# Optimization experiments

Hardware: AMD Instinct MI355X
Metric: run time of the kernel (lower is better)

Reference implementation:

```python
import jax, jax.numpy as jnp
import numpy as np

EPS = 1e-9

def setup_inputs() -> dict:
    key = jax.random.key(0)
    ks = jax.random.split(key, 6)
    B, S, D, F, E, K = 2, 2048, 1024, 4096, 8, 2
    hidden = jax.random.normal(ks[0], (B, S, D), dtype=jnp.float32)
    expert_indices = jax.random.randint(ks[1], (B, S, K), 0, E, dtype=jnp.int32)
    expert_weights = jax.random.uniform(ks[2], (B, S, K), dtype=jnp.float32)
    # normalize like a real top-k router would
    expert_weights = expert_weights / jnp.sum(expert_weights, axis=-1, keepdims=True)
    router_logits = jax.random.normal(ks[3], (B, S, E), dtype=jnp.float32)
    w1 = jax.random.normal(ks[4], (E, D, F), dtype=jnp.float32) * (1.0 / np.sqrt(D))
    b1 = jnp.zeros((E, F), dtype=jnp.float32)
    w2 = jax.random.normal(ks[5], (E, F, D), dtype=jnp.float32) * (1.0 / np.sqrt(F))
    b2 = jnp.zeros((E, D), dtype=jnp.float32)
    return {"hidden": hidden, "expert_indices": expert_indices,
            "expert_weights": expert_weights, "router_logits": router_logits,
            "w1": w1, "b1": b1, "w2": w2, "b2": b2}

def reference(hidden, expert_indices, expert_weights, router_logits, w1, b1, w2, b2):
    # All-expert dense compute (faithful to torch.stack([expert(hidden) ...], dim=-2))
    # hidden: [B,S,D]; w1: [E,D,F]; w2: [E,F,D]
    h1 = jnp.einsum('bsd,edf->bsef', hidden, w1) + b1            # [B,S,E,F]
    h1 = jax.nn.gelu(h1)
    expert_outputs = jnp.einsum('bsef,efd->bsed', h1, w2) + b2   # [B,S,E,D]
    # gather selected experts along expert axis (torch.gather dim=-2)
    idx = expert_indices[..., None]                              # [B,S,K,1]
    selected = jnp.take_along_axis(expert_outputs, idx, axis=-2) # [B,S,K,D]
    mixed = jnp.sum(selected * expert_weights[..., None], axis=-2)  # [B,S,D]
    # observation stats
    route_probs = jax.nn.softmax(router_logits, axis=-1)
    log_p = jnp.log(jnp.clip(route_probs, EPS, None))
    route_entropy = jnp.mean(jnp.sum(-route_probs * log_p, axis=-1))
    top2 = jax.lax.top_k(route_probs, 2)[0]
    winner_margin = jnp.mean(top2[..., 0] - top2[..., -1])
    return (mixed, route_entropy, winner_margin)
```

## Files before the change

kernel.cpp:

```cpp
#include <hip/hip_runtime.h>
#include <stddef.h>
#include <stdint.h>

#define BDIM 2
#define SDIM 2048
#define DDIM 1024
#define FDIM 4096
#define ENUM 8
#define KSEL 2
#define TTOK (BDIM * SDIM)
#define PPAIR (TTOK * KSEL)
#define VOUT ((size_t)TTOK * DDIM)

typedef float f32x4 __attribute__((ext_vector_type(4)));
typedef short bf16x8 __attribute__((ext_vector_type(8)));
typedef unsigned short u16x8 __attribute__((ext_vector_type(8)));
typedef unsigned short u16x4 __attribute__((ext_vector_type(4)));

#define WAITV(N) asm volatile("s_waitcnt vmcnt(" #N ")" ::: "memory")
#define BARX() asm volatile("s_barrier" ::: "memory")

__device__ __forceinline__ unsigned short f2bf(float f) {
  unsigned int u = __float_as_uint(f);
  u += 0x7fffu + ((u >> 16) & 1u);
  return (unsigned short)(u >> 16);
}

__device__ __forceinline__ float gelu_tanh(float x) {
  float u = 0.7978845608028654f * (x + 0.044715f * x * x * x);
  float e = __expf(2.0f * u);
  float t = 1.0f - 2.0f / (e + 1.0f);
  return 0.5f * x * (1.0f + t);
}

__device__ __forceinline__ void gload16(const void* g, void* l) {
  __builtin_amdgcn_global_load_lds(
      (const __attribute__((address_space(1))) unsigned int*)g,
      (__attribute__((address_space(3))) unsigned int*)l, 16, 0, 0);
}

__global__ __launch_bounds__(256) void pre_kernel(const float* __restrict__ hidden,
                                                  unsigned short* __restrict__ hB,
                                                  const float* __restrict__ lg,
                                                  float* __restrict__ pst,
                                                  const int* __restrict__ eidx,
                                                  int* __restrict__ g_cnt,
                                                  int* __restrict__ g_off,
                                                  int* __restrict__ pairTok,
                                                  int* __restrict__ inv,
                                                  int* __restrict__ b256E,
                                                  int* __restrict__ b256M,
                                                  int* __restrict__ b128E,
                                                  int* __restrict__ b128M,
                                                  int* __restrict__ nT) {
  const int b = blockIdx.x;
  const int tid = threadIdx.x;
  if (b < 2048) {
    const int i = b * 256 + tid;
    f32x4 a = ((const f32x4*)hidden)[(size_t)i * 2];
    f32x4 c = ((const f32x4*)hidden)[(size_t)i * 2 + 1];
    u16x8 o;
    o[0] = f2bf(a[0]); o[1] = f2bf(a[1]); o[2] = f2bf(a[2]); o[3] = f2bf(a[3]);
    o[4] = f2bf(c[0]); o[5] = f2bf(c[1]); o[6] = f2bf(c[2]); o[7] = f2bf(c[3]);
    ((u16x8*)hB)[i] = o;
    return;
  }
  if (b < 2064) {
    __shared__ float se[256], sm[256];
    const int r = (b - 2048) * 256 + tid;
    float v[ENUM];
    float mx = -1e30f;
#pragma unroll
    for (int i = 0; i < ENUM; ++i) { v[i] = lg[r * ENUM + i]; mx = fmaxf(mx, v[i]); }
    float s = 0.f;
#pragma unroll
    for (int i = 0; i < ENUM; ++i) { v[i] = __expf(v[i] - mx); s += v[i]; }
    float invs = 1.f / s;
    float p1 = -1.f, p2 = -1.f, e_ = 0.f;
#pragma unroll
    for (int i = 0; i < ENUM; ++i) {
      float p = v[i] * invs;
      e_ -= p * logf(fmaxf(p, 1e-9f));
      if (p > p1) { p2 = p1; p1 = p; } else if (p > p2) { p2 = p; }
    }
    se[tid] = e_; sm[tid] = p1 - p2;
    __syncthreads();
    for (int st = 128; st > 0; st >>= 1) {
      if (tid < (unsigned)st) { se[tid] += se[tid + st]; sm[tid] += sm[tid + st]; }
      __syncthreads();
    }
    if (tid == 0) { pst[(b - 2048) * 2] = se[0]; pst[(b - 2048) * 2 + 1] = sm[0]; }
    return;
  }
  __shared__ int sc[ENUM], so[ENUM], scur[ENUM];
  if (tid < ENUM) sc[tid] = 0;
  __syncthreads();
  for (int p = tid; p < PPAIR; p += 256) atomicAdd(&sc[eidx[p]], 1);
  __syncthreads();
  if (tid == 0) {
    int o = 0, n256 = 0, n128 = 0;
    for (int e = 0; e < ENUM; ++e) {
      so[e] = o;
      const int cnt = sc[e];
      const int nf = cnt >> 8;
      const int rem = cnt - (nf << 8);
      for (int i = 0; i < nf; ++i) { b256E[n256] = e; b256M[n256] = i << 8; ++n256; }
      const int np = (rem + 127) >> 7;
      for (int j = 0; j < np; ++j) { b128E[n128] = e; b128M[n128] = (nf << 8) + (j << 7); ++n128; }
      o += cnt;
    }
    nT[0] = n256; nT[1] = n128;
  }
  __syncthreads();
  if (tid < ENUM) { scur[tid] = so[tid]; g_cnt[tid] = sc[tid]; g_off[tid] = so[tid]; }
  __syncthreads();
  for (int p = tid; p < PPAIR; p += 256) {
    int e = eidx[p];
    int pos = atomicAdd(&scur[e], 1);
    pairTok[pos] = p >> 1;
    inv[p] = pos;
  }
}

__global__ void statsB_kernel(const float* __restrict__ pst, float* __restrict__ out) {
  if (threadIdx.x == 0) {
    float a = 0.f, b = 0.f;
    for (int i = 0; i < 16; ++i) { a += pst[2 * i]; b += pst[2 * i + 1]; }
    out[VOUT]     = a / (float)TTOK;
    out[VOUT + 1] = b / (float)TTOK;
  }
}

__global__ __launch_bounds__(256) void transpose2_kernel(const float* __restrict__ w1,
                                                         unsigned short* __restrict__ w1T,
                                                         const float* __restrict__ w2,
                                                         unsigned short* __restrict__ w2T) {
  __shared__ float tile[64][65];
  const int z = blockIdx.y;
  const int b = blockIdx.x;
  const float* ip; unsigned short* op; int R, C, r0, c0;
  if (z < 8) {
    const size_t base = (size_t)z * DDIM * FDIM;
    ip = w1 + base; op = w1T + base; R = DDIM; C = FDIM;
    r0 = (b >> 6) << 6; c0 = (b & 63) << 6;
  } else {
    const size_t base = (size_t)(z - 8) * DDIM * FDIM;
    ip = w2 + base; op = w2T + base; R = FDIM; C = DDIM;
    r0 = (b & 63) << 6; c0 = (b >> 6) << 6;
  }
  const int tid = threadIdx.x;
  const int rr = tid >> 4;
  const int cc = (tid & 15) << 2;
#pragma unroll
  for (int k = 0; k < 4; ++k) {
    f32x4 v = *(const f32x4*)(ip + (size_t)(r0 + rr + 16 * k) * C + c0 + cc);
    tile[rr + 16 * k][cc + 0] = v[0];
    tile[rr + 16 * k][cc + 1] = v[1];
    tile[rr + 16 * k][cc + 2] = v[2];
    tile[rr + 16 * k][cc + 3] = v[3];
  }
  __syncthreads();
  const int oc = tid >> 3;
  const int ob = (tid & 7) << 3;
#pragma unroll
  for (int k = 0; k < 2; ++k) {
    const int c = oc + 32 * k;
    u16x8 o;
#pragma unroll
    for (int j = 0; j < 8; ++j) o[j] = f2bf(tile[ob + j][c]);
    *(u16x8*)(op + (size_t)(c0 + c) * R + r0 + ob) = o;
  }
}

__global__ __launch_bounds__(512, 2) void gemm1_fused(const unsigned short* __restrict__ hB,
                                                      const unsigned short* __restrict__ w1T,
                                                      const float* __restrict__ b1,
                                                      const int* __restrict__ g_cnt,
                                                      const int* __restrict__ g_off,
                                                      const int* __restrict__ pairTok,
                                                      const int* __restrict__ b256E,
                                                      const int* __restrict__ b256M,
                                                      const int* __restrict__ b128E,
                                                      const int* __restrict__ b128M,
                                                      const int* __restrict__ nT,
                                                      unsigned short* __restrict__ h1) {
  __shared__ __align__(16) char smem[131072];
  const int flat = blockIdx.x + 48 * blockIdx.y;
  const int w = (flat & 7) * 96 + (flat >> 3);
  const int mIdx = w % 48;
  const int nB = w / 48;
  const int n0 = nB << 8;

  const int tid = threadIdx.x;
  const int lane = tid & 63;
  const int wm = (tid >> 6) >> 2;
  const int wn = (tid >> 6) & 3;
  const int kh = lane >> 4;
  const int l15 = lane & 15;

  if (mIdx < 32) {
    if (mIdx >= nT[0]) return;
    const int e = b256E[mIdx];
    const int m0 = b256M[mIdx];
    const int off_e = g_off[e];

    const unsigned short* gArow[2];
    const unsigned short* gBrow[2];
    int ldsOff[2];
#pragma unroll
    for (int c = 0; c < 2; ++c) {
      const int idx = c * 512 + tid;
      const int row = idx >> 2;
      const int g = (idx & 3) ^ ((row >> 1) & 3);
      ldsOff[c] = idx * 16;
      const int tok = pairTok[off_e + m0 + row];
      gArow[c] = hB + (size_t)tok * DDIM + g * 8;
      gBrow[c] = w1T + ((size_t)e * FDIM + (n0 + row)) * DDIM + g * 8;
    }

#define AH_OFF(bufv, ksv) (((bufv) * 2 + (ksv)) * 16384)
#define BH_OFF(bufv, ksv) (65536 + ((bufv) * 2 + (ksv)) * 16384)
#define G1_STAGE_A(bufv, ksv, kofs) do { \
    gload16(gArow[0] + (kofs), smem + AH_OFF(bufv, ksv) + ldsOff[0]); \
    gload16(gArow[1] + (kofs), smem + AH_OFF(bufv, ksv) + ldsOff[1]); } while (0)
#define G1_STAGE_B(bufv, ksv, kofs) do { \
    gload16(gBrow[0] + (kofs), smem + BH_OFF(bufv, ksv) + ldsOff[0]); \
    gload16(gBrow[1] + (kofs), smem + BH_OFF(bufv, ksv) + ldsOff[1]); } while (0)

    int aoff[8], boff[4];
#pragma unroll
    for (int i = 0; i < 8; ++i) {
      const int r = wm * 128 + i * 16 + l15;
      aoff[i] = r * 64 + ((kh ^ ((r >> 1) & 3)) << 4);
    }
#pragma unroll
    for (int i = 0; i < 4; ++i) {
      const int r = wn * 64 + i * 16 + l15;
      boff[i] = r * 64 + ((kh ^ ((r >> 1) & 3)) << 4);
    }

    f32x4 acc[8][4];
#pragma unroll
    for (int i = 0; i < 8; ++i)
#pragma unroll
      for (int j = 0; j < 4; ++j) acc[i][j] = (f32x4){0.f, 0.f, 0.f, 0.f};

    const int KT = DDIM / 64;
    G1_STAGE_A(0, 0, 0);  G1_STAGE_B(0, 0, 0);
    G1_STAGE_A(0, 1, 32); G1_STAGE_B(0, 1, 32);
    G1_STAGE_A(1, 0, 64); G1_STAGE_B(1, 0, 64);
    G1_STAGE_A(1, 1, 96);
    WAITV(6);
    BARX();

    for (int t = 0; t < KT; ++t) {
      const int buf = t & 1;
      const int bufn = buf ^ 1;
      const int ko1 = (t + 1) * 64;
      const int ko2 = (t + 2) * 64;
      bf16x8 af[4], bv[4];
#pragma unroll
      for (int ks = 0; ks < 2; ++ks) {
#pragma unroll
        for (int i = 0; i < 4; ++i) bv[i] = *(const bf16x8*)(smem + BH_OFF(buf, ks) + boff[i]);
#pragma unroll
        for (int i = 0; i < 4; ++i) af[i] = *(const bf16x8*)(smem + AH_OFF(buf, ks) + aoff[i]);
        __builtin_amdgcn_s_setprio(1);
#pragma unroll
        for (int mi = 0; mi < 4; ++mi)
#pragma unroll
          for (int ni = 0; ni < 4; ++ni)
            acc[mi][ni] = __builtin_amdgcn_mfma_f32_16x16x32_bf16(af[mi], bv[ni], acc[mi][ni], 0, 0, 0);
        __builtin_amdgcn_s_setprio(0);
        if (ks == 0) { if (t + 1 < KT) G1_STAGE_B(bufn, 1, ko1 + 32); }
        else         { if (t + 2 < KT) G1_STAGE_B(buf, 0, ko2); }
        BARX();
#pragma unroll
        for (int i = 0; i < 4; ++i) af[i] = *(const bf16x8*)(smem + AH_OFF(buf, ks) + aoff[4 + i]);
        __builtin_amdgcn_s_setprio(1);
#pragma unroll
        for (int mi = 0; mi < 4; ++mi)
#pragma unroll
          for (int ni = 0; ni < 4; ++ni)
            acc[4 + mi][ni] = __builtin_amdgcn_mfma_f32_16x16x32_bf16(af[mi], bv[ni], acc[4 + mi][ni], 0, 0, 0);
        __builtin_amdgcn_s_setprio(0);
        if (ks == 0) { if (t + 2 < KT) G1_STAGE_A(buf, 0, ko2); }
        else {
          if (t + 2 < KT) G1_STAGE_A(buf, 1, ko2 + 32);
          if (t < KT - 2)      { WAITV(6); }
          else if (t == KT - 2){ WAITV(0); }
        }
        BARX();
      }
    }
#undef G1_STAGE_A
#undef G1_STAGE_B
#undef AH_OFF
#undef BH_OFF

    float bias[4];
#pragma unroll
    for (int ni = 0; ni < 4; ++ni)
      bias[ni] = b1[e * FDIM + n0 + wn * 64 + ni * 16 + l15];
#pragma unroll
    for (int mi = 0; mi < 8; ++mi) {
#pragma unroll
      for (int j = 0; j < 4; ++j) {
        const int row = wm * 128 + mi * 16 + kh * 4 + j;
        unsigned short* dst = h1 + (size_t)(off_e + m0 + row) * FDIM + n0 + wn * 64;
#pragma unroll
        for (int ni = 0; ni < 4; ++ni)
          dst[ni * 16 + l15] = f2bf(gelu_tanh(acc[mi][ni][j] + bias[ni]));
      }
    }
    return;
  }

  {
    const int mI = mIdx - 32;
    if (mI >= nT[1]) return;
    const int e = b128E[mI];
    const int m0 = b128M[mI];
    const int off_e = g_off[e];
    const int rows_e = min(128, g_cnt[e] - m0);

    unsigned short* As = (unsigned short*)smem;
    unsigned short* Bs = (unsigned short*)(smem + 32768);
    const int ABUF = 128 * 64;
    const int BBUF = 256 * 64;

    const unsigned short* gA[2];
    const unsigned short* gB[4];
    int ldsA[2], ldsB[4];
#pragma unroll
    for (int c = 0; c < 2; ++c) {
      const int p = (c * 512 + tid) * 16;
      const int row = p >> 7;
      const int g = ((p >> 4) & 7) ^ (row & 7);
      ldsA[c] = p;
      const int tok = pairTok[off_e + m0 + min(row, rows_e - 1)];
      gA[c] = hB + (size_t)tok * DDIM + (g << 3);
    }
#pragma unroll
    for (int c = 0; c < 4; ++c) {
      const int p = (c * 512 + tid) * 16;
      const int row = p >> 7;
      const int g = ((p >> 4) & 7) ^ (row & 7);
      ldsB[c] = p;
      gB[c] = w1T + ((size_t)e * FDIM + (n0 + row)) * DDIM + (g << 3);
    }

    int aoff[4][2], boff[4][2];
#pragma unroll
    for (int i = 0; i < 4; ++i) {
      const int ar = wm * 64 + i * 16 + l15;
      const int br = wn * 64 + i * 16 + l15;
#pragma unroll
      for (int ks = 0; ks < 2; ++ks) {
        aoff[i][ks] = ar * 128 + ((((ks << 2) | kh) ^ (ar & 7)) << 4);
        boff[i][ks] = br * 128 + ((((ks << 2) | kh) ^ (br & 7)) << 4);
      }
    }

    f32x4 acc[4][4];
#pragma unroll
    for (int i = 0; i < 4; ++i)
#pragma unroll
      for (int j = 0; j < 4; ++j) acc[i][j] = (f32x4){0.f, 0.f, 0.f, 0.f};

#pragma unroll
    for (int c = 0; c < 2; ++c) gload16(gA[c], (char*)As + ldsA[c]);
#pragma unroll
    for (int c = 0; c < 4; ++c) gload16(gB[c], (char*)Bs + ldsB[c]);
    WAITV(0);
    BARX();

    int cur = 0;
    const int KT = DDIM / 64;
    for (int kt = 0; kt < KT; ++kt) {
      if (kt + 1 < KT) {
#pragma unroll
        for (int c = 0; c < 2; ++c) gload16(gA[c] + (size_t)(kt + 1) * 64, (char*)(As + (cur ^ 1) * ABUF) + ldsA[c]);
#pragma unroll
        for (int c = 0; c < 4; ++c) gload16(gB[c] + (size_t)(kt + 1) * 64, (char*)(Bs + (cur ^ 1) * BBUF) + ldsB[c]);
      }
#pragma unroll
      for (int ks = 0; ks < 2; ++ks) {
        bf16x8 af[4], bv[4];
#pragma unroll
        for (int i = 0; i < 4; ++i) af[i] = *(const bf16x8*)((const char*)(As + cur * ABUF) + aoff[i][ks]);
#pragma unroll
        for (int i = 0; i < 4; ++i) bv[i] = *(const bf16x8*)((const char*)(Bs + cur * BBUF) + boff[i][ks]);
        __builtin_amdgcn_s_setprio(1);
#pragma unroll
        for (int mi = 0; mi < 4; ++mi)
#pragma unroll
          for (int ni = 0; ni < 4; ++ni)
            acc[mi][ni] = __builtin_amdgcn_mfma_f32_16x16x32_bf16(af[mi], bv[ni], acc[mi][ni], 0, 0, 0);
        __builtin_amdgcn_s_setprio(0);
      }
      WAITV(0);
      BARX();
      cur ^= 1;
    }

    float bias[4];
#pragma unroll
    for (int ni = 0; ni < 4; ++ni)
      bias[ni] = b1[e * FDIM + n0 + wn * 64 + ni * 16 + l15];
#pragma unroll
    for (int mi = 0; mi < 4; ++mi) {
#pragma unroll
      for (int j = 0; j < 4; ++j) {
        const int row = wm * 64 + mi * 16 + kh * 4 + j;
        if (row < rows_e) {
          unsigned short* dst = h1 + (size_t)(off_e + m0 + row) * FDIM + n0 + wn * 64;
#pragma unroll
          for (int ni = 0; ni < 4; ++ni)
            dst[ni * 16 + l15] = f2bf(gelu_tanh(acc[mi][ni][j] + bias[ni]));
        }
      }
    }
  }
}

__global__ __launch_bounds__(512, 2) void gemm2_fused(const unsigned short* __restrict__ h1,
                                                      const unsigned short* __restrict__ w2T,
                                                      const float* __restrict__ b2,
                                                      const int* __restrict__ g_cnt,
                                                      const int* __restrict__ g_off,
                                                      const int* __restrict__ b256E,
                                                      const int* __restrict__ b256M,
                                                      const int* __restrict__ b128E,
                                                      const int* __restrict__ b128M,
                                                      const int* __restrict__ nT,
                                                      float* __restrict__ h2p) {
  __shared__ __align__(16) char smem[131072];
  const int flat = blockIdx.x + 48 * blockIdx.y + 192 * blockIdx.z;
  const int w = (flat & 7) * 48 + (flat >> 3);
  const int mIdx = w % 48;
  const int rest = w / 48;
  const int nB = rest & 3;
  const int s = rest >> 2;
  const int n0 = nB << 8;
  const int kbase = s * (FDIM / 2);

  const int tid = threadIdx.x;
  const int lane = tid & 63;
  const int wm = (tid >> 6) >> 2;
  const int wn = (tid >> 6) & 3;
  const int kh = lane >> 4;
  const int l15 = lane & 15;

  if (mIdx < 32) {
    if (mIdx >= nT[0]) return;
    const int e = b256E[mIdx];
    const int m0 = b256M[mIdx];
    const int off_e = g_off[e];

    const unsigned short* gArow[2];
    const unsigned short* gBrow[2];
    int ldsOff[2];
#pragma unroll
    for (int c = 0; c < 2; ++c) {
      const int idx = c * 512 + tid;
      const int row = idx >> 2;
      const int g = (idx & 3) ^ ((row >> 1) & 3);
      ldsOff[c] = idx * 16;
      gArow[c] = h1 + (size_t)(off_e + m0 + row) * FDIM + kbase + g * 8;
      gBrow[c] = w2T + ((size_t)e * DDIM + (n0 + row)) * FDIM + kbase + g * 8;
    }

#define AH_OFF(bufv, ksv) (((bufv) * 2 + (ksv)) * 16384)
#define BH_OFF(bufv, ksv) (65536 + ((bufv) * 2 + (ksv)) * 16384)
#define G2_STAGE_A(bufv, ksv, kofs) do { \
    gload16(gArow[0] + (kofs), smem + AH_OFF(bufv, ksv) + ldsOff[0]); \
    gload16(gArow[1] + (kofs), smem + AH_OFF(bufv, ksv) + ldsOff[1]); } while (0)
#define G2_STAGE_B(bufv, ksv, kofs) do { \
    gload16(gBrow[0] + (kofs), smem + BH_OFF(bufv, ksv) + ldsOff[0]); \
    gload16(gBrow[1] + (kofs), smem + BH_OFF(bufv, ksv) + ldsOff[1]); } while (0)

    int aoff[8], boff[4];
#pragma unroll
    for (int i = 0; i < 8; ++i) {
      const int r = wm * 128 + i * 16 + l15;
      aoff[i] = r * 64 + ((kh ^ ((r >> 1) & 3)) << 4);
    }
#pragma unroll
    for (int i = 0; i < 4; ++i) {
      const int r = wn * 64 + i * 16 + l15;
      boff[i] = r * 64 + ((kh ^ ((r >> 1) & 3)) << 4);
    }

    f32x4 acc[8][4];
#pragma unroll
    for (int i = 0; i < 8; ++i)
#pragma unroll
      for (int j = 0; j < 4; ++j) acc[i][j] = (f32x4){0.f, 0.f, 0.f, 0.f};

    const int KT = (FDIM / 2) / 64;
    G2_STAGE_A(0, 0, 0);  G2_STAGE_B(0, 0, 0);
    G2_STAGE_A(0, 1, 32); G2_STAGE_B(0, 1, 32);
    G2_STAGE_A(1, 0, 64); G2_STAGE_B(1, 0, 64);
    G2_STAGE_A(1, 1, 96);
    WAITV(6);
    BARX();

    for (int t = 0; t < KT; ++t) {
      const int buf = t & 1;
      const int bufn = buf ^ 1;
      const int ko1 = (t + 1) * 64;
      const int ko2 = (t + 2) * 64;
      bf16x8 af[4], bv[4];
#pragma unroll
      for (int ks = 0; ks < 2; ++ks) {
#pragma unroll
        for (int i = 0; i < 4; ++i) bv[i] = *(const bf16x8*)(smem + BH_OFF(buf, ks) + boff[i]);
#pragma unroll
        for (int i = 0; i < 4; ++i) af[i] = *(const bf16x8*)(smem + AH_OFF(buf, ks) + aoff[i]);
        __builtin_amdgcn_s_setprio(1);
#pragma unroll
        for (int mi = 0; mi < 4; ++mi)
#pragma unroll
          for (int ni = 0; ni < 4; ++ni)
            acc[mi][ni] = __builtin_amdgcn_mfma_f32_16x16x32_bf16(af[mi], bv[ni], acc[mi][ni], 0, 0, 0);
        __builtin_amdgcn_s_setprio(0);
        if (ks == 0) { if (t + 1 < KT) G2_STAGE_B(bufn, 1, ko1 + 32); }
        else         { if (t + 2 < KT) G2_STAGE_B(buf, 0, ko2); }
        BARX();
#pragma unroll
        for (int i = 0; i < 4; ++i) af[i] = *(const bf16x8*)(smem + AH_OFF(buf, ks) + aoff[4 + i]);
        __builtin_amdgcn_s_setprio(1);
#pragma unroll
        for (int mi = 0; mi < 4; ++mi)
#pragma unroll
          for (int ni = 0; ni < 4; ++ni)
            acc[4 + mi][ni] = __builtin_amdgcn_mfma_f32_16x16x32_bf16(af[mi], bv[ni], acc[4 + mi][ni], 0, 0, 0);
        __builtin_amdgcn_s_setprio(0);
        if (ks == 0) { if (t + 2 < KT) G2_STAGE_A(buf, 0, ko2); }
        else {
          if (t + 2 < KT) G2_STAGE_A(buf, 1, ko2 + 32);
          if (t < KT - 2)      { WAITV(6); }
          else if (t == KT - 2){ WAITV(0); }
        }
        BARX();
      }
    }
#undef G2_STAGE_A
#undef G2_STAGE_B
#undef AH_OFF
#undef BH_OFF

    float* outBase = h2p + (size_t)s * PPAIR * DDIM;
#pragma unroll
    for (int mi = 0; mi < 8; ++mi) {
#pragma unroll
      for (int j = 0; j < 4; ++j) {
        const int row = wm * 128 + mi * 16 + kh * 4 + j;
        float* dp = outBase + (size_t)(off_e + m0 + row) * DDIM;
#pragma unroll
        for (int ni = 0; ni < 4; ++ni) {
          const int col = n0 + wn * 64 + ni * 16 + l15;
          float v = acc[mi][ni][j];
          if (s == 0) v += b2[e * DDIM + col];
          dp[col] = v;
        }
      }
    }
    return;
  }

  {
    const int mI = mIdx - 32;
    if (mI >= nT[1]) return;
    const int e = b128E[mI];
    const int m0 = b128M[mI];
    const int off_e = g_off[e];
    const int rows_e = min(128, g_cnt[e] - m0);

    unsigned short* As = (unsigned short*)smem;
    unsigned short* Bs = (unsigned short*)(smem + 32768);
    const int ABUF = 128 * 64;
    const int BBUF = 256 * 64;

    const unsigned short* gA[2];
    const unsigned short* gB[4];
    int ldsA[2], ldsB[4];
#pragma unroll
    for (int c = 0; c < 2; ++c) {
      const int p = (c * 512 + tid) * 16;
      const int row = p >> 7;
      const int g = ((p >> 4) & 7) ^ (row & 7);
      ldsA[c] = p;
      gA[c] = h1 + (size_t)(off_e + m0 + min(row, rows_e - 1)) * FDIM + kbase + (g << 3);
    }
#pragma unroll
    for (int c = 0; c < 4; ++c) {
      const int p = (c * 512 + tid) * 16;
      const int row = p >> 7;
      const int g = ((p >> 4) & 7) ^ (row & 7);
      ldsB[c] = p;
      gB[c] = w2T + ((size_t)e * DDIM + (n0 + row)) * FDIM + kbase + (g << 3);
    }

    int aoff[4][2], boff[4][2];
#pragma unroll
    for (int i = 0; i < 4; ++i) {
      const int ar = wm * 64 + i * 16 + l15;
      const int br = wn * 64 + i * 16 + l15;
#pragma unroll
      for (int ks = 0; ks < 2; ++ks) {
        aoff[i][ks] = ar * 128 + ((((ks << 2) | kh) ^ (ar & 7)) << 4);
        boff[i][ks] = br * 128 + ((((ks << 2) | kh) ^ (br & 7)) << 4);
      }
    }

    f32x4 acc[4][4];
#pragma unroll
    for (int i = 0; i < 4; ++i)
#pragma unroll
      for (int j = 0; j < 4; ++j) acc[i][j] = (f32x4){0.f, 0.f, 0.f, 0.f};

#pragma unroll
    for (int c = 0; c < 2; ++c) gload16(gA[c], (char*)As + ldsA[c]);
#pragma unroll
    for (int c = 0; c < 4; ++c) gload16(gB[c], (char*)Bs + ldsB[c]);
    WAITV(0);
    BARX();

    int cur = 0;
    const int KT = (FDIM / 2) / 64;
    for (int kt = 0; kt < KT; ++kt) {
      if (kt + 1 < KT) {
#pragma unroll
        for (int c = 0; c < 2; ++c) gload16(gA[c] + (size_t)(kt + 1) * 64, (char*)(As + (cur ^ 1) * ABUF) + ldsA[c]);
#pragma unroll
        for (int c = 0; c < 4; ++c) gload16(gB[c] + (size_t)(kt + 1) * 64, (char*)(Bs + (cur ^ 1) * BBUF) + ldsB[c]);
      }
#pragma unroll
      for (int ks = 0; ks < 2; ++ks) {
        bf16x8 af[4], bv[4];
#pragma unroll
        for (int i = 0; i < 4; ++i) af[i] = *(const bf16x8*)((const char*)(As + cur * ABUF) + aoff[i][ks]);
#pragma unroll
        for (int i = 0; i < 4; ++i) bv[i] = *(const bf16x8*)((const char*)(Bs + cur * BBUF) + boff[i][ks]);
        __builtin_amdgcn_s_setprio(1);
#pragma unroll
        for (int mi = 0; mi < 4; ++mi)
#pragma unroll
          for (int ni = 0; ni < 4; ++ni)
            acc[mi][ni] = __builtin_amdgcn_mfma_f32_16x16x32_bf16(af[mi], bv[ni], acc[mi][ni], 0, 0, 0);
        __builtin_amdgcn_s_setprio(0);
      }
      WAITV(0);
      BARX();
      cur ^= 1;
    }

    float* outBase = h2p + (size_t)s * PPAIR * DDIM;
#pragma unroll
    for (int mi = 0; mi < 4; ++mi) {
#pragma unroll
      for (int j = 0; j < 4; ++j) {
        const int row = wm * 64 + mi * 16 + kh * 4 + j;
        if (row < rows_e) {
          float* dp = outBase + (size_t)(off_e + m0 + row) * DDIM;
#pragma unroll
          for (int ni = 0; ni < 4; ++ni) {
            const int col = n0 + wn * 64 + ni * 16 + l15;
            float v = acc[mi][ni][j];
            if (s == 0) v += b2[e * DDIM + col];
            dp[col] = v;
          }
        }
      }
    }
  }
}

__global__ __launch_bounds__(256) void combine_kernel(const float* __restrict__ h2p,
                                                      const float* __restrict__ ew,
                                                      const int* __restrict__ inv,
                                                      float* __restrict__ out) {
  const int i = blockIdx.x * 256 + threadIdx.x;
  const int t = i >> 8;
  const int c = i & 255;
  const int q0 = inv[t * 2], q1 = inv[t * 2 + 1];
  const float wa = ew[t * 2], wb = ew[t * 2 + 1];
  const f32x4* p0 = (const f32x4*)h2p;
  const f32x4* p1 = (const f32x4*)(h2p + (size_t)PPAIR * DDIM);
  f32x4 r = (p0[(size_t)q0 * 256 + c] + p1[(size_t)q0 * 256 + c]) * wa
          + (p0[(size_t)q1 * 256 + c] + p1[(size_t)q1 * 256 + c]) * wb;
  ((f32x4*)out)[i] = r;
}

extern "C" void kernel_launch(void* const* d_in, const int* in_sizes, int n_in,
                              void* d_out, int out_size, void* d_ws, size_t ws_size,
                              hipStream_t stream) {
  (void)in_sizes; (void)n_in; (void)out_size; (void)ws_size;
  const float* hidden = (const float*)d_in[0];
  const int*   eidx   = (const int*)d_in[1];
  const float* ew     = (const float*)d_in[2];
  const float* rlog   = (const float*)d_in[3];
  const float* w1     = (const float*)d_in[4];
  const float* b1     = (const float*)d_in[5];
  const float* w2     = (const float*)d_in[6];
  const float* b2     = (const float*)d_in[7];
  float* out = (float*)d_out;

  char* wsb = (char*)d_ws;
  const size_t SZ_W = (size_t)ENUM * DDIM * FDIM * 2;
  unsigned short* w1T = (unsigned short*)(wsb);
  unsigned short* w2T = (unsigned short*)(wsb + SZ_W);
  unsigned short* hB  = (unsigned short*)(wsb + 2 * SZ_W);
  unsigned short* h1  = (unsigned short*)(wsb + 2 * SZ_W + (size_t)TTOK * DDIM * 2);
  int* g_cnt   = (int*)(wsb + 2 * SZ_W + (size_t)TTOK * DDIM * 2 + (size_t)PPAIR * FDIM * 2);
  int* g_off   = g_cnt + 8;
  int* pairTok = g_off + 8;
  int* inv     = pairTok + PPAIR;
  int* b256E   = inv + PPAIR;
  int* b256M   = b256E + 32;
  int* b128E   = b256M + 32;
  int* b128M   = b128E + 16;
  int* nT      = b128M + 16;
  float* pstats = (float*)(nT + 2);
  float* h2p = (float*)wsb;

  pre_kernel<<<2065, 256, 0, stream>>>(hidden, hB, rlog, pstats, eidx, g_cnt, g_off,
                                       pairTok, inv, b256E, b256M, b128E, b128M, nT);
  statsB_kernel<<<1, 64, 0, stream>>>(pstats, out);
  transpose2_kernel<<<dim3(1024, 16), 256, 0, stream>>>(w1, w1T, w2, w2T);
  gemm1_fused<<<dim3(48, 16), 512, 0, stream>>>(hB, w1T, b1, g_cnt, g_off, pairTok,
                                                b256E, b256M, b128E, b128M, nT, h1);
  gemm2_fused<<<dim3(48, 4, 2), 512, 0, stream>>>(h1, w2T, b2, g_cnt, g_off,
                                                  b256E, b256M, b128E, b128M, nT, h2p);
  combine_kernel<<<(TTOK * DDIM / 4) / 256, 256, 0, stream>>>(h2p, ew, inv, out);
}
```

Baseline: 325.8 us.

## Fold weight transposes into pre_kernel and gemm1 launches to overlap work

```diff
diff --git a/kernel.cpp b/kernel.cpp
--- a/kernel.cpp
+++ b/kernel.cpp
@@ -52,7 +52,9 @@
                                                   int* __restrict__ b256M,
                                                   int* __restrict__ b128E,
                                                   int* __restrict__ b128M,
-                                                  int* __restrict__ nT) {
+                                                  int* __restrict__ nT,
+                                                  const float* __restrict__ w1,
+                                                  unsigned short* __restrict__ w1T) {
   const int b = blockIdx.x;
   const int tid = threadIdx.x;
   if (b < 2048) {
@@ -92,33 +94,68 @@
     if (tid == 0) { pst[(b - 2048) * 2] = se[0]; pst[(b - 2048) * 2 + 1] = sm[0]; }
     return;
   }
-  __shared__ int sc[ENUM], so[ENUM], scur[ENUM];
-  if (tid < ENUM) sc[tid] = 0;
-  __syncthreads();
-  for (int p = tid; p < PPAIR; p += 256) atomicAdd(&sc[eidx[p]], 1);
-  __syncthreads();
-  if (tid == 0) {
-    int o = 0, n256 = 0, n128 = 0;
-    for (int e = 0; e < ENUM; ++e) {
-      so[e] = o;
-      const int cnt = sc[e];
-      const int nf = cnt >> 8;
-      const int rem = cnt - (nf << 8);
-      for (int i = 0; i < nf; ++i) { b256E[n256] = e; b256M[n256] = i << 8; ++n256; }
-      const int np = (rem + 127) >> 7;
-      for (int j = 0; j < np; ++j) { b128E[n128] = e; b128M[n128] = (nf << 8) + (j << 7); ++n128; }
-      o += cnt;
-    }
-    nT[0] = n256; nT[1] = n128;
-  }
-  __syncthreads();
-  if (tid < ENUM) { scur[tid] = so[tid]; g_cnt[tid] = sc[tid]; g_off[tid] = so[tid]; }
-  __syncthreads();
-  for (int p = tid; p < PPAIR; p += 256) {
-    int e = eidx[p];
-    int pos = atomicAdd(&scur[e], 1);
-    pairTok[pos] = p >> 1;
-    inv[p] = pos;
+  if (b == 2064) {
+    __shared__ int sc[ENUM], so[ENUM], scur[ENUM];
+    if (tid < ENUM) sc[tid] = 0;
+    __syncthreads();
+    for (int p = tid; p < PPAIR; p += 256) atomicAdd(&sc[eidx[p]], 1);
+    __syncthreads();
+    if (tid == 0) {
+      int o = 0, n256 = 0, n128 = 0;
+      for (int e = 0; e < ENUM; ++e) {
+        so[e] = o;
+        const int cnt = sc[e];
+        const int nf = cnt >> 8;
+        const int rem = cnt - (nf << 8);
+        for (int i = 0; i < nf; ++i) { b256E[n256] = e; b256M[n256] = i << 8; ++n256; }
+        const int np = (rem + 127) >> 7;
+        for (int j = 0; j < np; ++j) { b128E[n128] = e; b128M[n128] = (nf << 8) + (j << 7); ++n128; }
+        o += cnt;
+      }
+      nT[0] = n256; nT[1] = n128;
+    }
+    __syncthreads();
+    if (tid < ENUM) { scur[tid] = so[tid]; g_cnt[tid] = sc[tid]; g_off[tid] = so[tid]; }
+    __syncthreads();
+    for (int p = tid; p < PPAIR; p += 256) {
+      int e = eidx[p];
+      int pos = atomicAdd(&scur[e], 1);
+      pairTok[pos] = p >> 1;
+      inv[p] = pos;
+    }
+    return;
+  }
+  {
+    __shared__ float tile[64][65];
+    const int t = b - 2065;
+    const int z = t >> 10;
+    const int bb = t & 1023;
+    const size_t base = (size_t)z * DDIM * FDIM;
+    const float* ip = w1 + base;
+    unsigned short* op = w1T + base;
+    const int r0 = (bb >> 6) << 6;
+    const int c0 = (bb & 63) << 6;
+    const int rr = tid >> 4;
+    const int cc = (tid & 15) << 2;
+#pragma unroll
+    for (int k = 0; k < 4; ++k) {
+      f32x4 v = *(const f32x4*)(ip + (size_t)(r0 + rr + 16 * k) * FDIM + c0 + cc);
+      tile[rr + 16 * k][cc + 0] = v[0];
+      tile[rr + 16 * k][cc + 1] = v[1];
+      tile[rr + 16 * k][cc + 2] = v[2];
+      tile[rr + 16 * k][cc + 3] = v[3];
+    }
+    __syncthreads();
+    const int oc = tid >> 3;
+    const int ob = (tid & 7) << 3;
+#pragma unroll
+    for (int k = 0; k < 2; ++k) {
+      const int c = oc + 32 * k;
+      u16x8 o;
+#pragma unroll
+      for (int j = 0; j < 8; ++j) o[j] = f2bf(tile[ob + j][c]);
+      *(u16x8*)(op + (size_t)(c0 + c) * DDIM + r0 + ob) = o;
+    }
   }
 }
 
@@ -128,47 +165,6 @@
     for (int i = 0; i < 16; ++i) { a += pst[2 * i]; b += pst[2 * i + 1]; }
     out[VOUT]     = a / (float)TTOK;
     out[VOUT + 1] = b / (float)TTOK;
-  }
-}
-
-__global__ __launch_bounds__(256) void transpose2_kernel(const float* __restrict__ w1,
-                                                         unsigned short* __restrict__ w1T,
-                                                         const float* __restrict__ w2,
-                                                         unsigned short* __restrict__ w2T) {
-  __shared__ float tile[64][65];
-  const int z = blockIdx.y;
-  const int b = blockIdx.x;
-  const float* ip; unsigned short* op; int R, C, r0, c0;
-  if (z < 8) {
-    const size_t base = (size_t)z * DDIM * FDIM;
-    ip = w1 + base; op = w1T + base; R = DDIM; C = FDIM;
-    r0 = (b >> 6) << 6; c0 = (b & 63) << 6;
-  } else {
-    const size_t base = (size_t)(z - 8) * DDIM * FDIM;
-    ip = w2 + base; op = w2T + base; R = FDIM; C = DDIM;
-    r0 = (b & 63) << 6; c0 = (b >> 6) << 6;
-  }
-  const int tid = threadIdx.x;
-  const int rr = tid >> 4;
-  const int cc = (tid & 15) << 2;
-#pragma unroll
-  for (int k = 0; k < 4; ++k) {
-    f32x4 v = *(const f32x4*)(ip + (size_t)(r0 + rr + 16 * k) * C + c0 + cc);
-    tile[rr + 16 * k][cc + 0] = v[0];
-    tile[rr + 16 * k][cc + 1] = v[1];
-    tile[rr + 16 * k][cc + 2] = v[2];
-    tile[rr + 16 * k][cc + 3] = v[3];
-  }
-  __syncthreads();
-  const int oc = tid >> 3;
-  const int ob = (tid & 7) << 3;
-#pragma unroll
-  for (int k = 0; k < 2; ++k) {
-    const int c = oc + 32 * k;
-    u16x8 o;
-#pragma unroll
-    for (int j = 0; j < 8; ++j) o[j] = f2bf(tile[ob + j][c]);
-    *(u16x8*)(op + (size_t)(c0 + c) * R + r0 + ob) = o;
   }
 }
 
@@ -183,15 +179,51 @@
                                                       const int* __restrict__ b128E,
                                                       const int* __restrict__ b128M,
                                                       const int* __restrict__ nT,
-                                                      unsigned short* __restrict__ h1) {
+                                                      unsigned short* __restrict__ h1,
+                                                      const float* __restrict__ w2,
+                                                      unsigned short* __restrict__ w2T) {
   __shared__ __align__(16) char smem[131072];
+  const int tid = threadIdx.x;
+
+  if (blockIdx.y >= 16) {
+    const int t = blockIdx.x + 48 * (blockIdx.y - 16);
+    if (t >= 8192) return;
+    float* tile = (float*)smem;
+    const int z = t >> 10;
+    const int bb = t & 1023;
+    const size_t base = (size_t)z * DDIM * FDIM;
+    const float* ip = w2 + base;
+    unsigned short* op = w2T + base;
+    const int r0 = (bb & 63) << 6;
+    const int c0 = (bb >> 6) << 6;
+    const int rr = tid >> 3;
+    const int cc8 = (tid & 7) << 3;
+    {
+      const float* src = ip + (size_t)(r0 + rr) * DDIM + c0 + cc8;
+      f32x4 v0 = *(const f32x4*)(src);
+      f32x4 v1 = *(const f32x4*)(src + 4);
+      float* tr = tile + rr * 65 + cc8;
+      tr[0] = v0[0]; tr[1] = v0[1]; tr[2] = v0[2]; tr[3] = v0[3];
+      tr[4] = v1[0]; tr[5] = v1[1]; tr[6] = v1[2]; tr[7] = v1[3];
+    }
+    __syncthreads();
+    {
+      const int oc = tid >> 3;
+      const int ob = (tid & 7) << 3;
+      u16x8 o;
+#pragma unroll
+      for (int j = 0; j < 8; ++j) o[j] = f2bf(tile[(ob + j) * 65 + oc]);
+      *(u16x8*)(op + (size_t)(c0 + oc) * FDIM + r0 + ob) = o;
+    }
+    return;
+  }
+
   const int flat = blockIdx.x + 48 * blockIdx.y;
   const int w = (flat & 7) * 96 + (flat >> 3);
   const int mIdx = w % 48;
   const int nB = w / 48;
   const int n0 = nB << 8;
 
-  const int tid = threadIdx.x;
   const int lane = tid & 63;
   const int wm = (tid >> 6) >> 2;
   const int wn = (tid >> 6) & 3;
@@ -726,12 +758,13 @@
   float* pstats = (float*)(nT + 2);
   float* h2p = (float*)wsb;
 
-  pre_kernel<<<2065, 256, 0, stream>>>(hidden, hB, rlog, pstats, eidx, g_cnt, g_off,
-                                       pairTok, inv, b256E, b256M, b128E, b128M, nT);
+  pre_kernel<<<2065 + 8192, 256, 0, stream>>>(hidden, hB, rlog, pstats, eidx, g_cnt, g_off,
+                                              pairTok, inv, b256E, b256M, b128E, b128M, nT,
+                                              w1, w1T);
   statsB_kernel<<<1, 64, 0, stream>>>(pstats, out);
-  transpose2_kernel<<<dim3(1024, 16), 256, 0, stream>>>(w1, w1T, w2, w2T);
-  gemm1_fused<<<dim3(48, 16), 512, 0, stream>>>(hB, w1T, b1, g_cnt, g_off, pairTok,
-                                                b256E, b256M, b128E, b128M, nT, h1);
+  gemm1_fused<<<dim3(48, 16 + 171), 512, 0, stream>>>(hB, w1T, b1, g_cnt, g_off, pairTok,
+                                                      b256E, b256M, b128E, b128M, nT, h1,
+                                                      w2, w2T);
   gemm2_fused<<<dim3(48, 4, 2), 512, 0, stream>>>(h1, w2T, b2, g_cnt, g_off,
                                                   b256E, b256M, b128E, b128M, nT, h2p);
   combine_kernel<<<(TTOK * DDIM / 4) / 256, 256, 0, stream>>>(h2p, ew, inv, out);
```

Result: no change. 320.6 us (-1.6%).
